# Performance work log

Hardware: AMD Instinct MI355X
Metric: run time of the kernel (lower is better)

## Reference

```python
import math
import jax, jax.numpy as jnp
import numpy as np

S, D = 4096, 2048
H, DH = 16, 128
ROPE_BASE = 10000.0


def _rotate_half(x):
    # x: [..., dh]; pairs (x1, x2) -> (-x2, x1), interleaved
    shp = x.shape
    x = x.reshape(*shp[:-1], shp[-1] // 2, 2)
    x1, x2 = x[..., 0], x[..., 1]
    return jnp.stack((-x2, x1), axis=-1).reshape(shp)


def _rope_cos_sin(seq_len, dh):
    inv_freq = 1.0 / (ROPE_BASE ** (jnp.arange(0, dh, 2, dtype=jnp.float32) / dh))
    t = jnp.arange(seq_len, dtype=jnp.float32)
    freqs = jnp.einsum('i,j->ij', t, inv_freq)  # [S, dh/2]
    cos = jnp.repeat(jnp.cos(freqs), 2, axis=-1)  # [S, dh]
    sin = jnp.repeat(jnp.sin(freqs), 2, axis=-1)
    return cos, sin


def setup_inputs() -> dict:
    key = jax.random.key(0)
    kx, kq, kk, kv, ko = jax.random.split(key, 5)
    scale_in = 1.0 / math.sqrt(D)
    scale_hd = 1.0 / math.sqrt(H * DH)
    return {
        'x': jax.random.normal(kx, (S, D), dtype=jnp.float32),
        'mask': jnp.tril(jnp.ones((S, S), dtype=bool)),  # causal
        'wq': jax.random.normal(kq, (H * DH, D), dtype=jnp.float32) * scale_in,
        'wk': jax.random.normal(kk, (H * DH, D), dtype=jnp.float32) * scale_in,
        'wv': jax.random.normal(kv, (H * DH, D), dtype=jnp.float32) * scale_in,
        'wo': jax.random.normal(ko, (D, H * DH), dtype=jnp.float32) * scale_hd,
    }


def reference(x, mask, wq, wk, wv, wo):
    s = x.shape[0]
    # QKV projections (Linear: y = W @ x per token) -> [h, S, dh]
    q = (x @ wq.T).reshape(s, H, DH).transpose(1, 0, 2)
    k = (x @ wk.T).reshape(s, H, DH).transpose(1, 0, 2)
    v = (x @ wv.T).reshape(s, H, DH).transpose(1, 0, 2)
    # RoPE
    cos, sin = _rope_cos_sin(s, DH)  # [S, dh] each
    q = q * cos[None] + _rotate_half(q) * sin[None]
    k = k * cos[None] + _rotate_half(k) * sin[None]
    # Attention
    sim = jnp.einsum('hid,hjd->hij', q, k) / math.sqrt(DH)  # [h, S, S]
    sim = jnp.where(mask[None], sim, -jnp.inf)
    attn = jax.nn.softmax(sim, axis=-1)
    out = jnp.einsum('hij,hjd->ihd', attn, v).reshape(s, H * DH)
    return out @ wo.T
```

## Files before the change

kernel.cpp:

```cpp
#include <hip/hip_runtime.h>
#include <stdint.h>

#define S_LEN 4096
#define D_MODEL 2048
#define NH 16
#define DH 128

typedef short s16x8 __attribute__((ext_vector_type(8)));
typedef short s16x2 __attribute__((ext_vector_type(2)));
typedef unsigned short u16;
typedef unsigned short u16x4 __attribute__((ext_vector_type(4)));
typedef float f32x4 __attribute__((ext_vector_type(4)));

__device__ __forceinline__ u16 f2bf(float f) {
  union { float f; uint32_t u; } v; v.f = f;
  uint32_t u = v.u;
  u += 0x7FFFu + ((u >> 16) & 1u);
  return (u16)(u >> 16);
}

__device__ __forceinline__ float bf2f(u16 b) {
  union { uint32_t u; float f; } v; v.u = ((uint32_t)b) << 16;
  return v.f;
}

__device__ __forceinline__ void async_copy16(const u16* g, u16* l) {
  __builtin_amdgcn_global_load_lds(
      (const __attribute__((address_space(1))) unsigned int*)g,
      (__attribute__((address_space(3))) unsigned int*)l, 16, 0, 0);
}

__global__ void cast_kernel(const float4* __restrict__ src, u16* __restrict__ dst, int n4) {
  int i = blockIdx.x * blockDim.x + threadIdx.x;
  if (i >= n4) return;
  float4 v = src[i];
  u16x4 o;
  o[0] = f2bf(v.x); o[1] = f2bf(v.y); o[2] = f2bf(v.z); o[3] = f2bf(v.w);
  *(u16x4*)(dst + (size_t)i * 4) = o;
}

__global__ void cast4_kernel(const float4* __restrict__ s0, const float4* __restrict__ s1,
                             const float4* __restrict__ s2, const float4* __restrict__ s3,
                             u16* __restrict__ d0, u16* __restrict__ d1,
                             u16* __restrict__ d2, u16* __restrict__ d3) {
  int b = blockIdx.x;
  int which = b >> 12;
  const float4* src = which == 0 ? s0 : which == 1 ? s1 : which == 2 ? s2 : s3;
  u16* dst = which == 0 ? d0 : which == 1 ? d1 : which == 2 ? d2 : d3;
  int i = (b & 4095) * blockDim.x + threadIdx.x;
  float4 v = src[i];
  u16x4 o;
  o[0] = f2bf(v.x); o[1] = f2bf(v.y); o[2] = f2bf(v.z); o[3] = f2bf(v.w);
  *(u16x4*)(dst + (size_t)i * 4) = o;
}

__global__ void rope_table(float* __restrict__ ctab, float* __restrict__ stab) {
  int idx = blockIdx.x * blockDim.x + threadIdx.x;
  int t = idx >> 6, p = idx & 63;
  float invf = powf(10000.0f, -(float)p / 64.0f);
  float th = (float)t * invf;
  ctab[idx] = cosf(th);
  stab[idx] = sinf(th);
}

__global__ __launch_bounds__(256) void gemm_qkv(
    const u16* __restrict__ A,
    const u16* __restrict__ wqb, const u16* __restrict__ wkb, const u16* __restrict__ wvb,
    u16* __restrict__ qh, u16* __restrict__ kh, u16* __restrict__ vh,
    const float* __restrict__ ctab, const float* __restrict__ stab)
{
  __shared__ __align__(16) u16 la[128 * 64];
  __shared__ __align__(16) u16 lb[128 * 64];
  const int tid = threadIdx.x;
  const int w = tid >> 6, lane = tid & 63, quad = lane >> 4, l16 = lane & 15;
  const int wm = (w & 1) << 6, wn = (w >> 1) << 6;
  const int m0 = blockIdx.x << 7;
  const int n0g = blockIdx.y << 7;
  const int which = n0g >> 11;
  const int n0 = n0g & 2047;
  const u16* B = which == 0 ? wqb : which == 1 ? wkb : wvb;
  u16* outp = which == 0 ? qh : which == 1 ? kh : vh;
  const int K = D_MODEL;

  f32x4 zero = {0.f, 0.f, 0.f, 0.f};
  f32x4 acc[4][4];
#pragma unroll
  for (int i = 0; i < 4; ++i)
#pragma unroll
    for (int j = 0; j < 4; ++j) acc[i][j] = zero;

  for (int k0 = 0; k0 < K; k0 += 64) {
    __syncthreads();
#pragma unroll
    for (int rnd = 0; rnd < 4; ++rnd) {
      int c = rnd * 256 + w * 64 + lane;
      int r = c >> 3, cc = c & 7;
      int gcol = ((cc ^ (r & 7)) << 3);
      int base = (rnd * 256 + w * 64) << 3;
      async_copy16(A + (size_t)(m0 + r) * K + k0 + gcol, la + base);
      async_copy16(B + (size_t)(n0 + r) * K + k0 + gcol, lb + base);
    }
    __syncthreads();
#pragma unroll
    for (int ks = 0; ks < 2; ++ks) {
      s16x8 af[4], bfr[4];
#pragma unroll
      for (int t = 0; t < 4; ++t) {
        int rowa = wm + (t << 4) + l16;
        af[t] = *(const s16x8*)(la + (rowa << 6) + ((((ks << 2) + quad) ^ (rowa & 7)) << 3));
        int rowb = wn + (t << 4) + l16;
        bfr[t] = *(const s16x8*)(lb + (rowb << 6) + ((((ks << 2) + quad) ^ (rowb & 7)) << 3));
      }
#pragma unroll
      for (int mt = 0; mt < 4; ++mt)
#pragma unroll
        for (int nt = 0; nt < 4; ++nt)
          acc[mt][nt] = __builtin_amdgcn_mfma_f32_16x16x32_bf16(af[mt], bfr[nt], acc[mt][nt], 0, 0, 0);
    }
  }

#pragma unroll
  for (int mt = 0; mt < 4; ++mt) {
    int rowg = m0 + wm + (mt << 4) + (quad << 2);
#pragma unroll
    for (int nt = 0; nt < 4; ++nt) {
      int cl = n0 + wn + (nt << 4) + l16;
      int hh = cl >> 7, dd = cl & 127;
      int p = dd >> 1;
      f32x4 v = acc[mt][nt];
#pragma unroll
      for (int r = 0; r < 4; ++r) {
        float val = v[r];
        if (which < 2) {
          float partner = __shfl_xor(val, 1);
          float c = ctab[(size_t)(rowg + r) * 64 + p];
          float s = stab[(size_t)(rowg + r) * 64 + p];
          val = (dd & 1) ? fmaf(val, c, partner * s) : fmaf(val, c, -partner * s);
        }
        outp[((size_t)hh * S_LEN + (rowg + r)) * DH + dd] = f2bf(val);
      }
    }
  }
}

__global__ __launch_bounds__(256) void gemm_bf16(
    const u16* __restrict__ A, const u16* __restrict__ B,
    float* __restrict__ outF, int M, int N, int K)
{
  __shared__ __align__(16) u16 la[128 * 64];
  __shared__ __align__(16) u16 lb[128 * 64];
  const int tid = threadIdx.x;
  const int w = tid >> 6, lane = tid & 63, quad = lane >> 4, l16 = lane & 15;
  const int wm = (w & 1) << 6, wn = (w >> 1) << 6;
  const int m0 = blockIdx.x << 7, n0 = blockIdx.y << 7;

  f32x4 zero = {0.f, 0.f, 0.f, 0.f};
  f32x4 acc[4][4];
#pragma unroll
  for (int i = 0; i < 4; ++i)
#pragma unroll
    for (int j = 0; j < 4; ++j) acc[i][j] = zero;

  for (int k0 = 0; k0 < K; k0 += 64) {
    __syncthreads();
#pragma unroll
    for (int rnd = 0; rnd < 4; ++rnd) {
      int c = rnd * 256 + w * 64 + lane;
      int r = c >> 3, cc = c & 7;
      int gcol = ((cc ^ (r & 7)) << 3);
      int base = (rnd * 256 + w * 64) << 3;
      async_copy16(A + (size_t)(m0 + r) * K + k0 + gcol, la + base);
      async_copy16(B + (size_t)(n0 + r) * K + k0 + gcol, lb + base);
    }
    __syncthreads();
#pragma unroll
    for (int ks = 0; ks < 2; ++ks) {
      s16x8 af[4], bfr[4];
#pragma unroll
      for (int t = 0; t < 4; ++t) {
        int rowa = wm + (t << 4) + l16;
        af[t] = *(const s16x8*)(la + (rowa << 6) + ((((ks << 2) + quad) ^ (rowa & 7)) << 3));
        int rowb = wn + (t << 4) + l16;
        bfr[t] = *(const s16x8*)(lb + (rowb << 6) + ((((ks << 2) + quad) ^ (rowb & 7)) << 3));
      }
#pragma unroll
      for (int mt = 0; mt < 4; ++mt)
#pragma unroll
        for (int nt = 0; nt < 4; ++nt)
          acc[mt][nt] = __builtin_amdgcn_mfma_f32_16x16x32_bf16(af[mt], bfr[nt], acc[mt][nt], 0, 0, 0);
    }
  }

#pragma unroll
  for (int mt = 0; mt < 4; ++mt) {
    int rowg = m0 + wm + (mt << 4) + (quad << 2);
#pragma unroll
    for (int nt = 0; nt < 4; ++nt) {
      int col = n0 + wn + (nt << 4) + l16;
      f32x4 v = acc[mt][nt];
#pragma unroll
      for (int r = 0; r < 4; ++r) outF[(size_t)(rowg + r) * N + col] = v[r];
    }
  }
}

__global__ __launch_bounds__(512) void attn_kernel(
    const u16* __restrict__ Q, const u16* __restrict__ Kb,
    const u16* __restrict__ V,
    u16* __restrict__ U0, u16* __restrict__ U1, float* __restrict__ lbuf)
{
  __shared__ __align__(16) u16 lk[64 * 128];
  __shared__ __align__(16) u16 lvt[128 * 64];

  const int tid = threadIdx.x;
  const int w = tid >> 6, lane = tid & 63, quad = lane >> 4, l16 = lane & 15;
  const int h = blockIdx.y;
  const int bx = blockIdx.x;

  const u16* Qh = Q + (size_t)h * S_LEN * DH;
  const u16* Kh = Kb + (size_t)h * S_LEN * DH;
  const u16* Vh = V + (size_t)h * S_LEN * DH;

  const float scale = 0.08838834764831845f;
  const s16x8 vones = {0x3F80, 0x3F80, 0x3F80, 0x3F80, 0x3F80, 0x3F80, 0x3F80, 0x3F80};
  f32x4 zero = {0.f, 0.f, 0.f, 0.f};

  for (int seg = 0; seg < 2; ++seg) {
    const int qt = seg ? bx : (31 - bx);
    const int jlo = seg ? (qt + 1) : 0;
    const int jhi = seg ? (2 * qt + 2) : (qt + 1);
    const int i0 = qt << 7;
    const int iw = i0 + (w << 4);

    s16x8 qf[4];
#pragma unroll
    for (int ks = 0; ks < 4; ++ks)
      qf[ks] = *(const s16x8*)(Qh + (size_t)(iw + l16) * DH + ks * 32 + quad * 8);

    f32x4 accO[8];
#pragma unroll
    for (int dt = 0; dt < 8; ++dt) accO[dt] = zero;
    f32x4 accL = zero;

    for (int jt = jlo; jt < jhi; ++jt) {
      const int j0 = jt << 6;
      __syncthreads();
#pragma unroll
      for (int rnd = 0; rnd < 2; ++rnd) {
        int c = rnd * 512 + tid;
        int r = c >> 4, cc = c & 15;
        int gcol = ((cc ^ (r & 15)) << 3);
        async_copy16(Kh + (size_t)(j0 + r) * DH + gcol, lk + ((rnd * 512 + w * 64) << 3));
      }
      {
        int u = tid & 31;
        int c8 = tid >> 5;
        int r0 = u << 1;
        s16x8 v0 = *(const s16x8*)(Vh + (size_t)(j0 + r0) * DH + (c8 << 3));
        s16x8 v1 = *(const s16x8*)(Vh + (size_t)(j0 + r0 + 1) * DH + (c8 << 3));
        int cc = r0 >> 3;
#pragma unroll
        for (int e = 0; e < 8; ++e) {
          int d = (c8 << 3) + e;
          int off = (d << 6) + ((cc ^ (d & 7)) << 3) + (r0 & 7);
          s16x2 pr = {v0[e], v1[e]};
          *(s16x2*)(lvt + off) = pr;
        }
      }
      __syncthreads();

      f32x4 sa[4];
#pragma unroll
      for (int nt = 0; nt < 4; ++nt) sa[nt] = zero;
#pragma unroll
      for (int ks = 0; ks < 4; ++ks) {
#pragma unroll
        for (int nt = 0; nt < 4; ++nt) {
          int row = (nt << 4) + l16;
          s16x8 kf = *(const s16x8*)(lk + (row << 7) + ((((ks << 2) + quad) ^ (row & 15)) << 3));
          sa[nt] = __builtin_amdgcn_mfma_f32_16x16x32_bf16(qf[ks], kf, sa[nt], 0, 0, 0);
        }
      }

      __syncthreads();

      const bool maskt = (j0 + 63 > iw);
      u16* lpw = lk + (w << 10);
#pragma unroll
      for (int nt = 0; nt < 4; ++nt) {
        int col = (nt << 4) + l16;
        int j = j0 + col;
        int ccp = col >> 3;
#pragma unroll
        for (int r = 0; r < 4; ++r) {
          float raw = sa[nt][r];
          if (maskt) {
            int i = iw + (quad << 2) + r;
            if (j > i) raw = -1.0e30f;
          }
          float p = __expf(fmaf(raw, scale, -8.0f));
          union { float f; uint32_t u; } pv; pv.f = p;
          int m = (quad << 2) + r;
          lpw[(m << 6) + ((ccp ^ (m & 7)) << 3) + (col & 7)] = (u16)(pv.u >> 16);
        }
      }
      asm volatile("s_waitcnt lgkmcnt(0)" ::: "memory");
      s16x8 pf[2];
#pragma unroll
      for (int kp = 0; kp < 2; ++kp)
        pf[kp] = *(const s16x8*)(lpw + (l16 << 6) + ((((kp << 2) + quad) ^ (l16 & 7)) << 3));

      accL = __builtin_amdgcn_mfma_f32_16x16x32_bf16(pf[0], vones, accL, 0, 0, 0);
      accL = __builtin_amdgcn_mfma_f32_16x16x32_bf16(pf[1], vones, accL, 0, 0, 0);

#pragma unroll
      for (int dt = 0; dt < 8; ++dt) {
#pragma unroll
        for (int kp = 0; kp < 2; ++kp) {
          int row = (dt << 4) + l16;
          s16x8 vf = *(const s16x8*)(lvt + (row << 6) + ((((kp << 2) + quad) ^ (row & 7)) << 3));
          accO[dt] = __builtin_amdgcn_mfma_f32_16x16x32_bf16(pf[kp], vf, accO[dt], 0, 0, 0);
        }
      }
    }

    u16* Useg = seg ? U1 : U0;
    float* ls = lbuf + (size_t)seg * NH * S_LEN + (size_t)h * S_LEN;
#pragma unroll
    for (int r = 0; r < 4; ++r) {
      float lr = accL[r];
      float inv = lr > 0.f ? 1.0f / lr : 0.f;
      int srow = iw + (quad << 2) + r;
#pragma unroll
      for (int dt = 0; dt < 8; ++dt)
        Useg[((size_t)h * S_LEN + srow) * DH + (dt << 4) + l16] = f2bf(accO[dt][r] * inv);
      if (l16 == 0) ls[srow] = lr;
    }
  }
}

__global__ void combine_kernel(const u16* __restrict__ U0, const u16* __restrict__ U1,
                               const float* __restrict__ lbuf, u16* __restrict__ ob)
{
  int t = blockIdx.x * 256 + threadIdx.x;
  int d8 = t & 15;
  int h = (t >> 4) & 15;
  int s = t >> 8;
  float l0 = lbuf[(size_t)h * S_LEN + s];
  float l1 = lbuf[(size_t)(NH * S_LEN) + (size_t)h * S_LEN + s];
  float inv = 1.0f / (l0 + l1);
  float w0 = l0 * inv, w1 = l1 * inv;
  size_t base = ((size_t)h * S_LEN + s) * DH + d8 * 8;
  s16x8 u0 = *(const s16x8*)(U0 + base);
  s16x8 u1 = *(const s16x8*)(U1 + base);
  u16 o[8];
#pragma unroll
  for (int e = 0; e < 8; ++e)
    o[e] = f2bf(w0 * bf2f((u16)u0[e]) + w1 * bf2f((u16)u1[e]));
  *(s16x8*)(ob + ((size_t)s * D_MODEL + h * DH + d8 * 8)) = *(s16x8*)o;
}

extern "C" void kernel_launch(void* const* d_in, const int* in_sizes, int n_in,
                              void* d_out, int out_size, void* d_ws, size_t ws_size,
                              hipStream_t stream) {
  const float* x  = (const float*)d_in[0];
  const float* wq = (const float*)d_in[2];
  const float* wk = (const float*)d_in[3];
  const float* wv = (const float*)d_in[4];
  const float* wo = (const float*)d_in[5];
  float* out = (float*)d_out;

  char* ws = (char*)d_ws;
  u16* xb  = (u16*)(ws);
  u16* wqb = (u16*)(ws + (16ull << 20));
  u16* wkb = (u16*)(ws + (24ull << 20));
  u16* wvb = (u16*)(ws + (32ull << 20));
  u16* wob = (u16*)(ws + (40ull << 20));
  u16* qh  = (u16*)(ws + (48ull << 20));
  u16* kh  = (u16*)(ws + (64ull << 20));
  u16* vh  = (u16*)(ws + (80ull << 20));
  float* ctab = (float*)(ws + (96ull << 20));
  float* stab = (float*)(ws + (97ull << 20));
  u16* U0 = (u16*)(ws);
  u16* U1 = (u16*)(ws + (16ull << 20));
  float* lbuf = (float*)(ws + (32ull << 20));
  u16* ob = qh;

  const int nx4 = S_LEN * D_MODEL / 4;
  cast_kernel<<<nx4 / 256, 256, 0, stream>>>((const float4*)x, xb, nx4);
  cast4_kernel<<<4 * 4096, 256, 0, stream>>>(
      (const float4*)wq, (const float4*)wk, (const float4*)wv, (const float4*)wo,
      wqb, wkb, wvb, wob);
  rope_table<<<(S_LEN * 64) / 256, 256, 0, stream>>>(ctab, stab);

  gemm_qkv<<<dim3(S_LEN / 128, 3 * D_MODEL / 128), 256, 0, stream>>>(
      xb, wqb, wkb, wvb, qh, kh, vh, ctab, stab);

  attn_kernel<<<dim3(32, NH), 512, 0, stream>>>(qh, kh, vh, U0, U1, lbuf);
  combine_kernel<<<S_LEN * NH * 16 / 256, 256, 0, stream>>>(U0, U1, lbuf, ob);

  gemm_bf16<<<dim3(S_LEN / 128, D_MODEL / 128), 256, 0, stream>>>(
      ob, wob, out, S_LEN, D_MODEL, D_MODEL);
}
```

Before: 525.3 us.

## Double-buffer K tiles and prefetch V into registers in attention loop

The attention kernel now keeps two K tiles in shared memory and issues the async copy for the next K tile, plus register loads of the next V tile, before computing on the current tile. The P scratch gets its own shared buffer instead of reusing the K tile, which removes the barrier between QK^T and the softmax. Barriers become raw s_waitcnt plus s_barrier sequences placed at the end of each iteration. The intent is to hide global memory latency behind MFMA work, at the cost of more LDS (roughly 64KB per block, which may lower occupancy) and more registers for the prefetched V data.

```diff
diff --git a/kernel.cpp b/kernel.cpp
--- a/kernel.cpp
+++ b/kernel.cpp
@@ -29,6 +29,9 @@
       (const __attribute__((address_space(1))) unsigned int*)g,
       (__attribute__((address_space(3))) unsigned int*)l, 16, 0, 0);
 }
+
+#define BAR_LGKM() asm volatile("s_waitcnt lgkmcnt(0)\n\ts_barrier" ::: "memory")
+#define BAR_FULL() asm volatile("s_waitcnt vmcnt(0) lgkmcnt(0)\n\ts_barrier" ::: "memory")
 
 __global__ void cast_kernel(const float4* __restrict__ src, u16* __restrict__ dst, int n4) {
   int i = blockIdx.x * blockDim.x + threadIdx.x;
@@ -209,8 +212,9 @@
     const u16* __restrict__ V,
     u16* __restrict__ U0, u16* __restrict__ U1, float* __restrict__ lbuf)
 {
-  __shared__ __align__(16) u16 lk[64 * 128];
+  __shared__ __align__(16) u16 lk[2][64 * 128];
   __shared__ __align__(16) u16 lvt[128 * 64];
+  __shared__ __align__(16) u16 lp[8][16 * 64];
 
   const int tid = threadIdx.x;
   const int w = tid >> 6, lane = tid & 63, quad = lane >> 4, l16 = lane & 15;
@@ -224,6 +228,8 @@
   const float scale = 0.08838834764831845f;
   const s16x8 vones = {0x3F80, 0x3F80, 0x3F80, 0x3F80, 0x3F80, 0x3F80, 0x3F80, 0x3F80};
   f32x4 zero = {0.f, 0.f, 0.f, 0.f};
+
+  const int vu = tid & 31, vc8 = tid >> 5, vr0 = vu << 1, vcc = vr0 >> 3;
 
   for (int seg = 0; seg < 2; ++seg) {
     const int qt = seg ? bx : (31 - bx);
@@ -242,32 +248,47 @@
     for (int dt = 0; dt < 8; ++dt) accO[dt] = zero;
     f32x4 accL = zero;
 
-    for (int jt = jlo; jt < jhi; ++jt) {
-      const int j0 = jt << 6;
-      __syncthreads();
+    {
+      const int j0 = jlo << 6;
 #pragma unroll
       for (int rnd = 0; rnd < 2; ++rnd) {
         int c = rnd * 512 + tid;
         int r = c >> 4, cc = c & 15;
         int gcol = ((cc ^ (r & 15)) << 3);
-        async_copy16(Kh + (size_t)(j0 + r) * DH + gcol, lk + ((rnd * 512 + w * 64) << 3));
-      }
-      {
-        int u = tid & 31;
-        int c8 = tid >> 5;
-        int r0 = u << 1;
-        s16x8 v0 = *(const s16x8*)(Vh + (size_t)(j0 + r0) * DH + (c8 << 3));
-        s16x8 v1 = *(const s16x8*)(Vh + (size_t)(j0 + r0 + 1) * DH + (c8 << 3));
-        int cc = r0 >> 3;
-#pragma unroll
-        for (int e = 0; e < 8; ++e) {
-          int d = (c8 << 3) + e;
-          int off = (d << 6) + ((cc ^ (d & 7)) << 3) + (r0 & 7);
-          s16x2 pr = {v0[e], v1[e]};
-          *(s16x2*)(lvt + off) = pr;
-        }
-      }
-      __syncthreads();
+        async_copy16(Kh + (size_t)(j0 + r) * DH + gcol, lk[0] + ((rnd * 512 + w * 64) << 3));
+      }
+      s16x8 v0 = *(const s16x8*)(Vh + (size_t)(j0 + vr0) * DH + (vc8 << 3));
+      s16x8 v1 = *(const s16x8*)(Vh + (size_t)(j0 + vr0 + 1) * DH + (vc8 << 3));
+#pragma unroll
+      for (int e = 0; e < 8; ++e) {
+        int d = (vc8 << 3) + e;
+        int off = (d << 6) + ((vcc ^ (d & 7)) << 3) + (vr0 & 7);
+        s16x2 pr = {v0[e], v1[e]};
+        *(s16x2*)(lvt + off) = pr;
+      }
+    }
+    BAR_FULL();
+
+    for (int jt = jlo; jt < jhi; ++jt) {
+      const int cur = (jt - jlo) & 1;
+      const int j0 = jt << 6;
+      const bool havenext = (jt + 1 < jhi);
+      const u16* lkc = lk[cur];
+
+      s16x8 vv0, vv1;
+      if (havenext) {
+        const int nj0 = (jt + 1) << 6;
+        vv0 = *(const s16x8*)(Vh + (size_t)(nj0 + vr0) * DH + (vc8 << 3));
+        vv1 = *(const s16x8*)(Vh + (size_t)(nj0 + vr0 + 1) * DH + (vc8 << 3));
+        u16* lkn = lk[cur ^ 1];
+#pragma unroll
+        for (int rnd = 0; rnd < 2; ++rnd) {
+          int c = rnd * 512 + tid;
+          int r = c >> 4, cc = c & 15;
+          int gcol = ((cc ^ (r & 15)) << 3);
+          async_copy16(Kh + (size_t)(nj0 + r) * DH + gcol, lkn + ((rnd * 512 + w * 64) << 3));
+        }
+      }
 
       f32x4 sa[4];
 #pragma unroll
@@ -277,15 +298,13 @@
 #pragma unroll
         for (int nt = 0; nt < 4; ++nt) {
           int row = (nt << 4) + l16;
-          s16x8 kf = *(const s16x8*)(lk + (row << 7) + ((((ks << 2) + quad) ^ (row & 15)) << 3));
+          s16x8 kf = *(const s16x8*)(lkc + (row << 7) + ((((ks << 2) + quad) ^ (row & 15)) << 3));
           sa[nt] = __builtin_amdgcn_mfma_f32_16x16x32_bf16(qf[ks], kf, sa[nt], 0, 0, 0);
         }
       }
 
-      __syncthreads();
-
       const bool maskt = (j0 + 63 > iw);
-      u16* lpw = lk + (w << 10);
+      u16* lpw = lp[w];
 #pragma unroll
       for (int nt = 0; nt < 4; ++nt) {
         int col = (nt << 4) + l16;
@@ -322,6 +341,18 @@
           accO[dt] = __builtin_amdgcn_mfma_f32_16x16x32_bf16(pf[kp], vf, accO[dt], 0, 0, 0);
         }
       }
+
+      if (havenext) {
+        BAR_LGKM();
+#pragma unroll
+        for (int e = 0; e < 8; ++e) {
+          int d = (vc8 << 3) + e;
+          int off = (d << 6) + ((vcc ^ (d & 7)) << 3) + (vr0 & 7);
+          s16x2 pr = {vv0[e], vv1[e]};
+          *(s16x2*)(lvt + off) = pr;
+        }
+        BAR_FULL();
+      }
     }
 
     u16* Useg = seg ? U1 : U0;
@@ -336,6 +367,7 @@
         Useg[((size_t)h * S_LEN + srow) * DH + (dt << 4) + l16] = f2bf(accO[dt][r] * inv);
       if (l16 == 0) ls[srow] = lr;
     }
+    __syncthreads();
   }
 }
 
```

Measured after the change: 529.4 us. Within noise of the previous version (+0.8%).
